# Optimization experiments

Hardware: AMD Instinct MI355X
Metric: run time of the kernel (lower is better)

## Reference

```python
import jax, jax.numpy as jnp
import numpy as np

D_MODEL = 1024
N_HEADS = 16
HEAD_DIM = D_MODEL // N_HEADS
EPS = 1e-6


def _phi(x):
    # elu(x) + 1 feature map
    return jax.nn.elu(x) + 1.0


def setup_inputs() -> dict:
    key = jax.random.key(0)
    ks = jax.random.split(key, 12)
    B, N, M = 4, 4096, 4096
    s = 1.0 / np.sqrt(D_MODEL)
    return {
        "queries": jax.random.normal(ks[0], (B, N, D_MODEL), jnp.float32),
        "keys": jax.random.normal(ks[1], (B, M, D_MODEL), jnp.float32),
        "values": jax.random.normal(ks[2], (B, M, D_MODEL), jnp.float32),
        "wq": jax.random.normal(ks[3], (D_MODEL, D_MODEL), jnp.float32) * s,
        "bq": jax.random.normal(ks[4], (D_MODEL,), jnp.float32) * s,
        "wk": jax.random.normal(ks[5], (D_MODEL, D_MODEL), jnp.float32) * s,
        "bk": jax.random.normal(ks[6], (D_MODEL,), jnp.float32) * s,
        "wv": jax.random.normal(ks[7], (D_MODEL, D_MODEL), jnp.float32) * s,
        "bv": jax.random.normal(ks[8], (D_MODEL,), jnp.float32) * s,
        "wo": jax.random.normal(ks[9], (D_MODEL, D_MODEL), jnp.float32) * s,
        "bo": jax.random.normal(ks[10], (D_MODEL,), jnp.float32) * s,
    }


def reference(queries, keys, values, wq, bq, wk, bk, wv, bv, wo, bo):
    B, N, _ = queries.shape
    M = keys.shape[1]
    H, Dh = N_HEADS, HEAD_DIM
    # projections + head split -> [B, H, seq, Dh]
    q = _phi((queries @ wq.T + bq).reshape(B, N, H, Dh).transpose(0, 2, 1, 3))
    k = _phi((keys @ wk.T + bk).reshape(B, M, H, Dh).transpose(0, 2, 1, 3))
    v = (values @ wv.T + bv).reshape(B, M, H, Dh).transpose(0, 2, 1, 3)
    # kv aggregation: [B,H,Dh,Dh]
    kv = jnp.einsum("bhmd,bhme->bhde", k, v)
    # normalizer: [B,H,Dh]
    z = k.sum(axis=2)
    num = jnp.einsum("bhnd,bhde->bhne", q, kv)
    den = jnp.einsum("bhnd,bhd->bhn", q, z)[..., None] + EPS
    out = (num / den).transpose(0, 2, 1, 3).reshape(B, N, H * Dh)
    return out @ wo.T + bo
```

## Files before the change

kernel.cpp:

```cpp
#include <hip/hip_runtime.h>

#define EPS 1e-6f

typedef __attribute__((ext_vector_type(8))) __bf16 bf16x8;
typedef __attribute__((ext_vector_type(4))) float f32x4;
typedef __attribute__((ext_vector_type(4))) unsigned short us4v;
typedef __attribute__((ext_vector_type(8))) unsigned short us8v;
typedef unsigned short us;

__device__ inline us f2bf(float f) {
  unsigned int u = __builtin_bit_cast(unsigned int, f);
  unsigned int r = (u + 0x7fffu + ((u >> 16) & 1u)) >> 16;
  return (us)r;
}
__device__ inline float bf2f(us s) {
  unsigned int u = ((unsigned int)s) << 16;
  return __builtin_bit_cast(float, u);
}

__device__ inline void gl_lds16(const us* g, us* l) {
  __builtin_amdgcn_global_load_lds(
      (const __attribute__((address_space(1))) unsigned int*)g,
      (__attribute__((address_space(3))) unsigned int*)l, 16, 0, 0);
}

__global__ __launch_bounds__(256) void conv_bf16(const float* __restrict__ s,
                                                 us* __restrict__ d) {
  int idx = blockIdx.x * 256 + threadIdx.x;
  size_t base = (size_t)idx * 8;
  float4 a = *(const float4*)(s + base);
  float4 b = *(const float4*)(s + base + 4);
  us8v o;
  o[0] = f2bf(a.x); o[1] = f2bf(a.y); o[2] = f2bf(a.z); o[3] = f2bf(a.w);
  o[4] = f2bf(b.x); o[5] = f2bf(b.y); o[6] = f2bf(b.z); o[7] = f2bf(b.w);
  *(us8v*)(d + base) = o;
}

template <int MODE>
__global__ __launch_bounds__(512, 2) void proj_gemm(const us* __restrict__ X,
                                                    const us* __restrict__ W,
                                                    const float* __restrict__ bias,
                                                    void* __restrict__ Yv) {
  __shared__ alignas(16) us As[4][256 * 32];
  __shared__ alignas(16) us Bs[4][256 * 32];

  const int t = threadIdx.x;
  const int wave = t >> 6, lane = t & 63;
  const int q4 = lane >> 4, l16 = lane & 15;
  const int wm = wave >> 2, wn = wave & 3;
  const int bid = blockIdx.x;
  const int rowg = (bid & 7) * 8 + (bid >> 5);
  const int colg = (bid >> 3) & 3;
  const int rowBase = rowg << 8;
  const int colBase = colg << 8;

  const int spos = (t & 3) ^ ((t >> 3) & 3);
  const us* Xg = X + (size_t)(rowBase + (t >> 2)) * 1024 + spos * 8;
  const us* Wg = W + (size_t)(colBase + (t >> 2)) * 1024 + spos * 8;
  const int cA = (q4 ^ ((l16 >> 1) & 3)) * 8;

  f32x4 acc[8][4];
#pragma unroll
  for (int i = 0; i < 8; i++)
#pragma unroll
    for (int j = 0; j < 4; j++) acc[i][j] = (f32x4){0.f, 0.f, 0.f, 0.f};

#define STAGEP(tt)                                                         \
  {                                                                        \
    const int k0_ = (tt) * 32;                                             \
    us* Ad_ = &As[(tt) & 3][wave * 64 * 8];                                \
    us* Bd_ = &Bs[(tt) & 3][wave * 64 * 8];                                \
    gl_lds16(Xg + k0_, Ad_);                                               \
    gl_lds16(Xg + (size_t)128 * 1024 + k0_, Ad_ + 512 * 8);                \
    gl_lds16(Wg + k0_, Bd_);                                               \
    gl_lds16(Wg + (size_t)128 * 1024 + k0_, Bd_ + 512 * 8);                \
  }

  STAGEP(0);
  STAGEP(1);
  STAGEP(2);

#pragma unroll 4
  for (int tt = 0; tt < 32; ++tt) {
    if (tt < 29) {
      STAGEP(tt + 3);
      asm volatile("s_waitcnt vmcnt(12)" ::: "memory");
    } else if (tt == 29) {
      asm volatile("s_waitcnt vmcnt(8)" ::: "memory");
    } else if (tt == 30) {
      asm volatile("s_waitcnt vmcnt(4)" ::: "memory");
    } else {
      asm volatile("s_waitcnt vmcnt(0)" ::: "memory");
    }
    asm volatile("s_barrier" ::: "memory");

    const us* Ab = &As[tt & 3][0];
    const us* Bb2 = &Bs[tt & 3][0];
    bf16x8 af[8], bfv[4];
#pragma unroll
    for (int i = 0; i < 8; i++)
      af[i] = *(const bf16x8*)&Ab[(wm * 128 + i * 16 + l16) * 32 + cA];
#pragma unroll
    for (int j = 0; j < 4; j++)
      bfv[j] = *(const bf16x8*)&Bb2[(wn * 64 + j * 16 + l16) * 32 + cA];

    __builtin_amdgcn_s_setprio(1);
#pragma unroll
    for (int i = 0; i < 8; i++)
#pragma unroll
      for (int j = 0; j < 4; j++)
        acc[i][j] = __builtin_amdgcn_mfma_f32_16x16x32_bf16(af[i], bfv[j],
                                                            acc[i][j], 0, 0, 0);
    __builtin_amdgcn_s_setprio(0);

    asm volatile("s_barrier" ::: "memory");
  }
#undef STAGEP

#pragma unroll
  for (int j = 0; j < 4; j++) {
    int col = colBase + wn * 64 + j * 16 + l16;
    float bv = bias[col];
#pragma unroll
    for (int i = 0; i < 8; i++) {
      int row0 = rowBase + wm * 128 + i * 16 + q4 * 4;
      if (MODE == 1 || MODE == 2) {
        int b = row0 >> 12, m0 = row0 & 4095;
        int h = col >> 6, dd = col & 63;
        us4v pk;
#pragma unroll
        for (int r = 0; r < 4; r++) {
          float y = acc[i][j][r] + bv;
          if (MODE == 1) y = (y > 0.f) ? (y + 1.f) : __expf(y);
          pk[r] = f2bf(y);
        }
        *(us4v*)&((us*)Yv)[(((size_t)((b * 16 + h) * 64 + dd)) << 12) + m0] = pk;
      } else {
#pragma unroll
        for (int r = 0; r < 4; r++) {
          float y = acc[i][j][r] + bv;
          if (MODE == 0) {
            y = (y > 0.f) ? (y + 1.f) : __expf(y);
            ((us*)Yv)[(size_t)(row0 + r) * 1024 + col] = f2bf(y);
          } else {
            ((float*)Yv)[(size_t)(row0 + r) * 1024 + col] = y;
          }
        }
      }
    }
  }
}

__global__ __launch_bounds__(256) void kv_stage1(const us* __restrict__ kt,
                                                 const us* __restrict__ vt,
                                                 float* __restrict__ part,
                                                 float* __restrict__ zpart) {
  __shared__ float red[4][4096];
  __shared__ float zred[4][64][4];

  const int blk = blockIdx.x;
  const int bh = blk >> 2, split = blk & 3;
  const int t = threadIdx.x;
  const int w = t >> 6, lane = t & 63;
  const int q4 = lane >> 4, l16 = lane & 15;
  const us* ktb = kt + (size_t)bh * 64 * 4096;
  const us* vtb = vt + (size_t)bh * 64 * 4096;
  const int mbeg = split * 1024 + w * 256;

  f32x4 acc[4][4];
#pragma unroll
  for (int i = 0; i < 4; i++)
#pragma unroll
    for (int j = 0; j < 4; j++) acc[i][j] = (f32x4){0.f, 0.f, 0.f, 0.f};
  float zacc[4] = {0.f, 0.f, 0.f, 0.f};

  for (int m0 = mbeg; m0 < mbeg + 256; m0 += 32) {
    bf16x8 af[4], bfr[4];
#pragma unroll
    for (int i = 0; i < 4; i++)
      af[i] = *(const bf16x8*)&vtb[(size_t)(i * 16 + l16) * 4096 + m0 + q4 * 8];
#pragma unroll
    for (int j = 0; j < 4; j++) {
      us8v ub = *(const us8v*)&ktb[(size_t)(j * 16 + l16) * 4096 + m0 + q4 * 8];
      bfr[j] = __builtin_bit_cast(bf16x8, ub);
#pragma unroll
      for (int e = 0; e < 8; e++) zacc[j] += bf2f(ub[e]);
    }
#pragma unroll
    for (int i = 0; i < 4; i++)
#pragma unroll
      for (int j = 0; j < 4; j++)
        acc[i][j] = __builtin_amdgcn_mfma_f32_16x16x32_bf16(af[i], bfr[j], acc[i][j], 0, 0, 0);
  }

#pragma unroll
  for (int i = 0; i < 4; i++)
#pragma unroll
    for (int j = 0; j < 4; j++)
#pragma unroll
      for (int r = 0; r < 4; r++)
        red[w][(i * 16 + q4 * 4 + r) * 64 + j * 16 + l16] = acc[i][j][r];
#pragma unroll
  for (int j = 0; j < 4; j++) zred[w][j * 16 + l16][q4] = zacc[j];
  __syncthreads();

  float* pb = part + (size_t)blk * 4096;
#pragma unroll
  for (int i = 0; i < 16; i++) {
    int idx = t + 256 * i;
    pb[idx] = red[0][idx] + red[1][idx] + red[2][idx] + red[3][idx];
  }
  if (t < 64) {
    float s = 0.f;
#pragma unroll
    for (int w2 = 0; w2 < 4; w2++)
#pragma unroll
      for (int q = 0; q < 4; q++) s += zred[w2][t][q];
    zpart[blk * 64 + t] = s;
  }
}

__global__ __launch_bounds__(256) void kv_stage2(const float* __restrict__ part,
                                                 const float* __restrict__ zpart,
                                                 us* __restrict__ kvb,
                                                 float* __restrict__ z) {
  const int bh = blockIdx.x;
  const int t = threadIdx.x;
  const float* p0 = part + (size_t)bh * 4 * 4096;
#pragma unroll
  for (int i = 0; i < 16; i++) {
    int idx = t + 256 * i;
    float s = p0[idx] + p0[4096 + idx] + p0[8192 + idx] + p0[12288 + idx];
    kvb[(size_t)bh * 4096 + idx] = f2bf(s);
  }
  if (t < 64) {
    const float* zp = zpart + (size_t)bh * 4 * 64;
    z[bh * 64 + t] = zp[t] + zp[64 + t] + zp[128 + t] + zp[192 + t];
  }
}

__global__ __launch_bounds__(256) void attn_kernel(const us* __restrict__ q,
                                                   const us* __restrict__ kvb,
                                                   const float* __restrict__ z,
                                                   us* __restrict__ attn) {
  __shared__ alignas(16) us kvs[64 * 72];
  __shared__ float zs[64];
  __shared__ float invden[256];

  const int bid = blockIdx.x;
  const int bh = bid >> 4, nc = bid & 15;
  const int b = bh >> 4, h = bh & 15;
  const int n0 = nc * 256;
  const int t = threadIdx.x;
  const int wave = t >> 6, lane = t & 63;
  const int q4 = lane >> 4, l16 = lane & 15;

#pragma unroll
  for (int i = 0; i < 2; i++) {
    int chunk = t + 256 * i;
    int e = chunk >> 3, d8 = chunk & 7;
    us8v vv = *(const us8v*)&kvb[(size_t)bh * 4096 + chunk * 8];
    *(us8v*)&kvs[e * 72 + d8 * 8] = vv;
  }
  if (t < 64) zs[t] = z[bh * 64 + t];
  __syncthreads();

  {
    const us* qrow = q + ((size_t)(b * 4096 + n0 + t)) * 1024 + h * 64;
    float s = 0.f;
#pragma unroll
    for (int d0 = 0; d0 < 64; d0 += 8) {
      us8v v = *(const us8v*)(qrow + d0);
#pragma unroll
      for (int j = 0; j < 8; j++) s += bf2f(v[j]) * zs[d0 + j];
    }
    invden[t] = 1.0f / (s + EPS);
  }
  __syncthreads();

  f32x4 acc[4][4];
#pragma unroll
  for (int i = 0; i < 4; i++)
#pragma unroll
    for (int j = 0; j < 4; j++) acc[i][j] = (f32x4){0.f, 0.f, 0.f, 0.f};

  const us* qb = q + ((size_t)(b * 4096 + n0 + wave * 64)) * 1024 + h * 64;
#pragma unroll
  for (int ks = 0; ks < 2; ks++) {
    bf16x8 af[4], bfr[4];
#pragma unroll
    for (int i = 0; i < 4; i++)
      af[i] = *(const bf16x8*)(qb + (size_t)(i * 16 + l16) * 1024 + ks * 32 + q4 * 8);
#pragma unroll
    for (int j = 0; j < 4; j++)
      bfr[j] = *(const bf16x8*)&kvs[(j * 16 + l16) * 72 + ks * 32 + q4 * 8];
#pragma unroll
    for (int i = 0; i < 4; i++)
#pragma unroll
      for (int j = 0; j < 4; j++)
        acc[i][j] = __builtin_amdgcn_mfma_f32_16x16x32_bf16(af[i], bfr[j], acc[i][j], 0, 0, 0);
  }

  us* ab = attn + ((size_t)(b * 4096 + n0 + wave * 64)) * 1024 + h * 64;
#pragma unroll
  for (int i = 0; i < 4; i++)
#pragma unroll
    for (int j = 0; j < 4; j++)
#pragma unroll
      for (int r = 0; r < 4; r++) {
        int rowl = i * 16 + q4 * 4 + r;
        int nl = wave * 64 + rowl;
        int e = j * 16 + l16;
        ab[(size_t)rowl * 1024 + e] = f2bf(acc[i][j][r] * invden[nl]);
      }
}

extern "C" void kernel_launch(void* const* d_in, const int* in_sizes, int n_in,
                              void* d_out, int out_size, void* d_ws, size_t ws_size,
                              hipStream_t stream) {
  const float* queries = (const float*)d_in[0];
  const float* keys    = (const float*)d_in[1];
  const float* values  = (const float*)d_in[2];
  const float* wq = (const float*)d_in[3];
  const float* bq = (const float*)d_in[4];
  const float* wk = (const float*)d_in[5];
  const float* bk = (const float*)d_in[6];
  const float* wv = (const float*)d_in[7];
  const float* bv = (const float*)d_in[8];
  const float* wo = (const float*)d_in[9];
  const float* bo = (const float*)d_in[10];

  char* ws = (char*)d_ws;
  const size_t TB = (size_t)16384 * 1024 * 2;
  us* A   = (us*)(ws);
  us* Bb  = (us*)(ws + TB);
  us* Xb  = (us*)(ws + 2 * TB);
  us* wqb = (us*)(ws + 3 * TB);
  us* wkb = wqb + (size_t)1024 * 1024;
  us* wvb = wkb + (size_t)1024 * 1024;
  us* wob = wvb + (size_t)1024 * 1024;
  float* part  = (float*)(wob + (size_t)1024 * 1024);
  float* zpart = part + (size_t)256 * 4096;
  float* z     = zpart + 256 * 64;
  us* kvb      = (us*)(z + 4096);

  const int GRID_IN = 16384 * 1024 / 2048;
  const int GRID_W  = 1024 * 1024 / 2048;

  conv_bf16<<<GRID_W, 256, 0, stream>>>(wq, wqb);
  conv_bf16<<<GRID_W, 256, 0, stream>>>(wk, wkb);
  conv_bf16<<<GRID_W, 256, 0, stream>>>(wv, wvb);
  conv_bf16<<<GRID_W, 256, 0, stream>>>(wo, wob);

  conv_bf16<<<GRID_IN, 256, 0, stream>>>(keys, Xb);
  proj_gemm<1><<<256, 512, 0, stream>>>(Xb, wkb, bk, (void*)A);
  conv_bf16<<<GRID_IN, 256, 0, stream>>>(values, Xb);
  proj_gemm<2><<<256, 512, 0, stream>>>(Xb, wvb, bv, (void*)Bb);
  kv_stage1<<<256, 256, 0, stream>>>(A, Bb, part, zpart);
  kv_stage2<<<64, 256, 0, stream>>>(part, zpart, kvb, z);
  conv_bf16<<<GRID_IN, 256, 0, stream>>>(queries, Bb);
  proj_gemm<0><<<256, 512, 0, stream>>>(Bb, wqb, bq, (void*)A);
  attn_kernel<<<1024, 256, 0, stream>>>(A, kvb, z, A);
  proj_gemm<3><<<256, 512, 0, stream>>>(A, wob, bo, d_out);
}
```

Measured before the change: 440.4 us.

## Restructure projection GEMM mainloop into K=64 double-buffered phased pipeline

Replaces the projection GEMM's 4-stage K=32 LDS pipeline with a 2-stage K=64 buffer using an 8-way XOR swizzle. Each K tile is split into four MFMA phases, and loads for the next A tile and the B tile two steps ahead are interleaved between phases with barriers and priority hints. The goal is fewer loop iterations and waits per unit of work and better overlap of global-to-LDS copies with MFMA. In exchange it adds more barriers per iteration and uses shallower prefetch, so memory latency may be exposed more often.

Result: no change. 442.2 us (+0.4%).

```diff
diff --git a/kernel.cpp b/kernel.cpp
--- a/kernel.cpp
+++ b/kernel.cpp
@@ -41,8 +41,8 @@
                                                     const us* __restrict__ W,
                                                     const float* __restrict__ bias,
                                                     void* __restrict__ Yv) {
-  __shared__ alignas(16) us As[4][256 * 32];
-  __shared__ alignas(16) us Bs[4][256 * 32];
+  __shared__ alignas(16) us As[2][256 * 64];
+  __shared__ alignas(16) us Bs[2][256 * 64];
 
   const int t = threadIdx.x;
   const int wave = t >> 6, lane = t & 63;
@@ -54,10 +54,15 @@
   const int rowBase = rowg << 8;
   const int colBase = colg << 8;
 
-  const int spos = (t & 3) ^ ((t >> 3) & 3);
-  const us* Xg = X + (size_t)(rowBase + (t >> 2)) * 1024 + spos * 8;
-  const us* Wg = W + (size_t)(colBase + (t >> 2)) * 1024 + spos * 8;
-  const int cA = (q4 ^ ((l16 >> 1) & 3)) * 8;
+  const int tr = t >> 3;
+  const int gsw = ((t & 7) ^ (tr & 7)) * 8;
+  const us* Xg = X + (size_t)(rowBase + tr) * 1024 + gsw;
+  const us* Wg = W + (size_t)(colBase + tr) * 1024 + gsw;
+
+  const int gx0 = ((0 | q4) ^ (l16 & 7)) * 8;
+  const int gx1 = ((4 | q4) ^ (l16 & 7)) * 8;
+  const int arow_off = (wm * 128 + l16) * 64;
+  const int brow_off = (wn * 64 + l16) * 64;
 
   f32x4 acc[8][4];
 #pragma unroll
@@ -65,57 +70,115 @@
 #pragma unroll
     for (int j = 0; j < 4; j++) acc[i][j] = (f32x4){0.f, 0.f, 0.f, 0.f};
 
-#define STAGEP(tt)                                                         \
-  {                                                                        \
-    const int k0_ = (tt) * 32;                                             \
-    us* Ad_ = &As[(tt) & 3][wave * 64 * 8];                                \
-    us* Bd_ = &Bs[(tt) & 3][wave * 64 * 8];                                \
-    gl_lds16(Xg + k0_, Ad_);                                               \
-    gl_lds16(Xg + (size_t)128 * 1024 + k0_, Ad_ + 512 * 8);                \
-    gl_lds16(Wg + k0_, Bd_);                                               \
-    gl_lds16(Wg + (size_t)128 * 1024 + k0_, Bd_ + 512 * 8);                \
-  }
-
-  STAGEP(0);
-  STAGEP(1);
-  STAGEP(2);
-
-#pragma unroll 4
-  for (int tt = 0; tt < 32; ++tt) {
-    if (tt < 29) {
-      STAGEP(tt + 3);
-      asm volatile("s_waitcnt vmcnt(12)" ::: "memory");
-    } else if (tt == 29) {
-      asm volatile("s_waitcnt vmcnt(8)" ::: "memory");
-    } else if (tt == 30) {
-      asm volatile("s_waitcnt vmcnt(4)" ::: "memory");
-    } else {
-      asm volatile("s_waitcnt vmcnt(0)" ::: "memory");
-    }
-    asm volatile("s_barrier" ::: "memory");
-
-    const us* Ab = &As[tt & 3][0];
-    const us* Bb2 = &Bs[tt & 3][0];
-    bf16x8 af[8], bfv[4];
-#pragma unroll
-    for (int i = 0; i < 8; i++)
-      af[i] = *(const bf16x8*)&Ab[(wm * 128 + i * 16 + l16) * 32 + cA];
-#pragma unroll
-    for (int j = 0; j < 4; j++)
-      bfv[j] = *(const bf16x8*)&Bb2[(wn * 64 + j * 16 + l16) * 32 + cA];
-
-    __builtin_amdgcn_s_setprio(1);
-#pragma unroll
-    for (int i = 0; i < 8; i++)
-#pragma unroll
-      for (int j = 0; j < 4; j++)
-        acc[i][j] = __builtin_amdgcn_mfma_f32_16x16x32_bf16(af[i], bfv[j],
-                                                            acc[i][j], 0, 0, 0);
-    __builtin_amdgcn_s_setprio(0);
-
-    asm volatile("s_barrier" ::: "memory");
-  }
-#undef STAGEP
+#define STAGE_A(kt, h)                                                      \
+  {                                                                         \
+    us* d_ = &As[(kt) & 1][((h) * 128 + wave * 8) * 64];                    \
+    const us* s_ = Xg + (size_t)((h) * 128) * 1024 + (kt) * 64;             \
+    gl_lds16(s_, d_);                                                       \
+    gl_lds16(s_ + (size_t)64 * 1024, d_ + 64 * 64);                         \
+  }
+#define STAGE_B(kt, h)                                                      \
+  {                                                                         \
+    us* d_ = &Bs[(kt) & 1][((h) * 128 + wave * 8) * 64];                    \
+    const us* s_ = Wg + (size_t)((h) * 128) * 1024 + (kt) * 64;             \
+    gl_lds16(s_, d_);                                                       \
+    gl_lds16(s_ + (size_t)64 * 1024, d_ + 64 * 64);                         \
+  }
+#define PH_SYNC_PRE()                                                       \
+  asm volatile("s_barrier" ::: "memory");                                   \
+  asm volatile("s_waitcnt lgkmcnt(0)" ::: "memory");                        \
+  __builtin_amdgcn_sched_barrier(0);                                        \
+  __builtin_amdgcn_s_setprio(1);
+#define PH_SYNC_POST()                                                      \
+  __builtin_amdgcn_s_setprio(0);                                           \
+  asm volatile("s_barrier" ::: "memory");
+#define MFMA16(J, AF)                                                       \
+  _Pragma("unroll") for (int s_i = 0; s_i < 2; ++s_i)                       \
+  _Pragma("unroll") for (int ks = 0; ks < 2; ++ks)                          \
+  _Pragma("unroll") for (int ni = 0; ni < 4; ++ni)                          \
+    acc[2 * (J) + s_i][ni] = __builtin_amdgcn_mfma_f32_16x16x32_bf16(       \
+        AF[s_i][ks], bfv[ni][ks], acc[2 * (J) + s_i][ni], 0, 0, 0);
+
+  STAGE_B(0, 0); STAGE_B(0, 1);
+  STAGE_A(0, 0); STAGE_A(0, 1);
+  STAGE_B(1, 0); STAGE_B(1, 1);
+  asm volatile("s_waitcnt vmcnt(4)" ::: "memory");
+  asm volatile("s_barrier" ::: "memory");
+
+#pragma unroll 2
+  for (int m = 0; m < 16; ++m) {
+    const int b = m & 1;
+    const us* Ar = &As[b][arow_off];
+    const us* Br = &Bs[b][brow_off];
+    bf16x8 bfv[4][2];
+
+    {
+      bf16x8 af[2][2];
+#pragma unroll
+      for (int s_i = 0; s_i < 2; ++s_i) {
+        af[s_i][0] = *(const bf16x8*)(Ar + (0 + s_i) * 1024 + gx0);
+        af[s_i][1] = *(const bf16x8*)(Ar + (0 + s_i) * 1024 + gx1);
+      }
+#pragma unroll
+      for (int ni = 0; ni < 4; ++ni) {
+        bfv[ni][0] = *(const bf16x8*)(Br + ni * 1024 + gx0);
+        bfv[ni][1] = *(const bf16x8*)(Br + ni * 1024 + gx1);
+      }
+      if (m < 15) STAGE_A(m + 1, 0);
+      PH_SYNC_PRE();
+      MFMA16(0, af);
+      PH_SYNC_POST();
+    }
+    {
+      bf16x8 af[2][2];
+#pragma unroll
+      for (int s_i = 0; s_i < 2; ++s_i) {
+        af[s_i][0] = *(const bf16x8*)(Ar + (2 + s_i) * 1024 + gx0);
+        af[s_i][1] = *(const bf16x8*)(Ar + (2 + s_i) * 1024 + gx1);
+      }
+      if (m < 15) STAGE_A(m + 1, 1);
+      PH_SYNC_PRE();
+      MFMA16(1, af);
+      PH_SYNC_POST();
+    }
+    {
+      bf16x8 af[2][2];
+#pragma unroll
+      for (int s_i = 0; s_i < 2; ++s_i) {
+        af[s_i][0] = *(const bf16x8*)(Ar + (4 + s_i) * 1024 + gx0);
+        af[s_i][1] = *(const bf16x8*)(Ar + (4 + s_i) * 1024 + gx1);
+      }
+      if (m < 14) STAGE_B(m + 2, 0);
+      PH_SYNC_PRE();
+      MFMA16(2, af);
+      PH_SYNC_POST();
+    }
+    {
+      bf16x8 af[2][2];
+#pragma unroll
+      for (int s_i = 0; s_i < 2; ++s_i) {
+        af[s_i][0] = *(const bf16x8*)(Ar + (6 + s_i) * 1024 + gx0);
+        af[s_i][1] = *(const bf16x8*)(Ar + (6 + s_i) * 1024 + gx1);
+      }
+      if (m < 14) STAGE_B(m + 2, 1);
+      asm volatile("s_barrier" ::: "memory");
+      asm volatile("s_waitcnt lgkmcnt(0)" ::: "memory");
+      __builtin_amdgcn_sched_barrier(0);
+      __builtin_amdgcn_s_setprio(1);
+      MFMA16(3, af);
+      __builtin_amdgcn_s_setprio(0);
+      if (m < 14)
+        asm volatile("s_waitcnt vmcnt(4)" ::: "memory");
+      else
+        asm volatile("s_waitcnt vmcnt(0)" ::: "memory");
+      asm volatile("s_barrier" ::: "memory");
+    }
+  }
+#undef STAGE_A
+#undef STAGE_B
+#undef PH_SYNC_PRE
+#undef PH_SYNC_POST
+#undef MFMA16
 
 #pragma unroll
   for (int j = 0; j < 4; j++) {
@@ -125,7 +188,7 @@
     for (int i = 0; i < 8; i++) {
       int row0 = rowBase + wm * 128 + i * 16 + q4 * 4;
       if (MODE == 1 || MODE == 2) {
-        int b = row0 >> 12, m0 = row0 & 4095;
+        int bb = row0 >> 12, m0 = row0 & 4095;
         int h = col >> 6, dd = col & 63;
         us4v pk;
 #pragma unroll
@@ -134,7 +197,7 @@
           if (MODE == 1) y = (y > 0.f) ? (y + 1.f) : __expf(y);
           pk[r] = f2bf(y);
         }
-        *(us4v*)&((us*)Yv)[(((size_t)((b * 16 + h) * 64 + dd)) << 12) + m0] = pk;
+        *(us4v*)&((us*)Yv)[(((size_t)((bb * 16 + h) * 64 + dd)) << 12) + m0] = pk;
       } else {
 #pragma unroll
         for (int r = 0; r < 4; r++) {
```
